# Kernel tuning notes

Measured on AMD Instinct MI355X. Metric: run time of the kernel, lower is better.

## Reference

```python
import jax, jax.numpy as jnp
import numpy as np

NUM_HEADS = 8
SIZES = [(80, 80), (40, 40), (20, 20), (10, 10), (5, 5)]


def _ln(x, g, b):
    m = x.mean(-1, keepdims=True)
    var = ((x - m) ** 2).mean(-1, keepdims=True)
    return (x - m) / jnp.sqrt(var + 1e-5) * g + b


def setup_inputs() -> dict:
    key = jax.random.key(0)
    ks = jax.random.split(key, 24)
    bs, c, S = 2, 256, 1024  # v_dim = embed_dim = c
    d = {}
    for i, (h, w) in enumerate(SIZES):
        d[f"q{i}"] = jax.random.normal(ks[i], (bs, c, h, w), jnp.float32)
    d["cache"] = jax.random.normal(ks[5], (bs, S, c), jnp.float32)
    d["mask"] = jax.random.randint(ks[6], (bs, S), 0, 2).astype(jnp.int32)
    d["ln_v_g"] = jnp.ones((c,), jnp.float32)
    d["ln_v_b"] = jnp.zeros((c,), jnp.float32)
    d["ln_c_g"] = jnp.ones((c,), jnp.float32)
    d["ln_c_b"] = jnp.zeros((c,), jnp.float32)
    sd = c ** -0.5
    d["Wv"] = jax.random.normal(ks[7], (c, c), jnp.float32) * sd
    d["bv"] = jnp.zeros((c,), jnp.float32)
    d["Wc"] = jax.random.normal(ks[8], (c, c), jnp.float32) * sd
    d["bc"] = jnp.zeros((c,), jnp.float32)
    d["Wvc"] = jax.random.normal(ks[9], (c, c), jnp.float32) * sd
    d["bvc"] = jnp.zeros((c,), jnp.float32)
    d["Wo"] = jax.random.normal(ks[10], (c, c), jnp.float32) * sd
    d["bo"] = jnp.zeros((c,), jnp.float32)
    d["Wg1"] = jax.random.normal(ks[11], (c, c // 2), jnp.float32) * sd
    d["bg1"] = jnp.zeros((c // 2,), jnp.float32)
    d["Wg2"] = jax.random.normal(ks[12], (c // 2, c), jnp.float32) * 0.01
    d["bg2"] = jnp.zeros((c,), jnp.float32)
    return d


def _forward(q0, q1, q2, q3, q4, cache, mask, ln_v_g, ln_v_b, ln_c_g, ln_c_b,
             Wv, bv, Wc, bc, Wvc, bvc, Wo, bo, Wg1, bg1, Wg2, bg2):
    feats = [q0, q1, q2, q3, q4]
    bs = q0.shape[0]
    sizes = [(f.shape[2], f.shape[3]) for f in feats]
    # permute_and_flatten: (bs, c, h, w) -> (bs, h*w, c), concat over levels
    v = jnp.concatenate(
        [f.reshape(bs, f.shape[1], -1).transpose(0, 2, 1) for f in feats], axis=1)
    T = v.shape[1]
    E = Wv.shape[1]
    hd = E // NUM_HEADS
    scale = hd ** -0.5

    vn = _ln(v, ln_v_g, ln_v_b)
    cn = _ln(cache, ln_c_g, ln_c_b)

    q = ((vn @ Wv + bv) * scale).reshape(bs, T, NUM_HEADS, hd).transpose(0, 2, 1, 3)
    k = (cn @ Wc + bc).reshape(bs, -1, NUM_HEADS, hd).transpose(0, 2, 1, 3)
    val = (cn @ Wvc + bvc).reshape(bs, -1, NUM_HEADS, hd).transpose(0, 2, 1, 3)

    attn = jnp.einsum('bhtd,bhsd->bhts', q, k)
    attn = jnp.clip(attn, -50000.0, 50000.0)
    mf = mask.astype(attn.dtype)  # (bs, S); zeros -> -9e15, ones kept as +1.0 (faithful)
    attn = attn + jnp.where(mf == 0, jnp.asarray(-9e15, attn.dtype), mf)[:, None, None, :]
    p = jax.nn.softmax(attn, axis=-1)  # dropout inactive in eval mode

    o = jnp.einsum('bhts,bhsd->bhtd', p, val).transpose(0, 2, 1, 3).reshape(bs, T, E)
    delta = o @ Wo + bo

    gate = jnp.tanh(jax.nn.relu(v @ Wg1 + bg1) @ Wg2 + bg2)
    new_v = (v + gate * delta).transpose(0, 2, 1)  # (bs, c, T)

    outs = []
    start = 0
    for h, w in sizes:
        outs.append(new_v[:, :, start:start + h * w].reshape(bs, -1, h, w))
        start += h * w
    return tuple(outs)


def reference(q0, q1, q2, q3, q4, cache, mask, ln_v_g, ln_v_b, ln_c_g, ln_c_b,
              Wv, bv, Wc, bc, Wvc, bvc, Wo, bo, Wg1, bg1, Wg2, bg2):
    return _forward(q0, q1, q2, q3, q4, cache, mask, ln_v_g, ln_v_b, ln_c_g, ln_c_b,
                    Wv, bv, Wc, bc, Wvc, bvc, Wo, bo, Wg1, bg1, Wg2, bg2)
```

## Files before the change

kernel.cpp:

```cpp
#include <hip/hip_runtime.h>
#include <hip/hip_bf16.h>
#include <math.h>


typedef __attribute__((ext_vector_type(8))) short short8;
typedef __attribute__((ext_vector_type(4))) float f32x4;
typedef __hip_bfloat16 bf16;

#define T_TOK 8525
#define S_TOK 1024
#define CDIM  256
#define NHEAD 8
#define BSZ   2

static __device__ __forceinline__ f32x4 mfma16(short8 a, short8 b, f32x4 c) {
  return __builtin_amdgcn_mfma_f32_16x16x32_bf16(a, b, c, 0, 0, 0);
}

__global__ __launch_bounds__(256) void prep_weights(
    const float* __restrict__ Wv, const float* __restrict__ Wc,
    const float* __restrict__ Wvc, const float* __restrict__ Wo,
    const float* __restrict__ Wg1, const float* __restrict__ Wg2,
    const float* __restrict__ bc, const float* __restrict__ bvc,
    bf16* __restrict__ WvT, bf16* __restrict__ WcvcT, bf16* __restrict__ WoT,
    bf16* __restrict__ Wg1T, bf16* __restrict__ Wg2T, float* __restrict__ biasCV) {
  const int bid = blockIdx.x, tid = threadIdx.x;
  if (bid >= 80) {
    biasCV[tid] = bc[tid];
    biasCV[tid + 256] = bvc[tid];
    return;
  }
  const float* W; bf16* WT; int K, N, local;
  if (bid < 16)      { W = Wv;  WT = WvT;           K = 256; N = 256; local = bid; }
  else if (bid < 32) { W = Wc;  WT = WcvcT;         K = 256; N = 256; local = bid - 16; }
  else if (bid < 48) { W = Wvc; WT = WcvcT + 65536; K = 256; N = 256; local = bid - 32; }
  else if (bid < 64) { W = Wo;  WT = WoT;           K = 256; N = 256; local = bid - 48; }
  else if (bid < 72) { W = Wg1; WT = Wg1T;          K = 256; N = 128; local = bid - 64; }
  else               { W = Wg2; WT = Wg2T;          K = 128; N = 256; local = bid - 72; }
  const int ktiles = K >> 6;
  const int K0 = (local % ktiles) * 64, N0 = (local / ktiles) * 64;
  __shared__ float tl[64][65];
  const int kk = tid >> 4, n4 = (tid & 15) * 4;
#pragma unroll
  for (int i = 0; i < 4; ++i) {
    int k = kk + 16 * i;
    float4 w4 = *(const float4*)&W[(size_t)(K0 + k) * N + N0 + n4];
    tl[n4 + 0][k] = w4.x; tl[n4 + 1][k] = w4.y;
    tl[n4 + 2][k] = w4.z; tl[n4 + 3][k] = w4.w;
  }
  __syncthreads();
  const int nn = tid >> 4, k4 = (tid & 15) * 4;
#pragma unroll
  for (int i = 0; i < 4; ++i) {
    int n = nn + 16 * i;
    bf16 o[4] __attribute__((aligned(8)));
#pragma unroll
    for (int j = 0; j < 4; ++j) o[j] = __float2bfloat16(tl[n][k4 + j]);
    *(uint2*)&WT[(size_t)(N0 + n) * K + K0 + k4] = *(uint2*)o;
  }
}

__global__ __launch_bounds__(256) void build_v_ln(
    const float* __restrict__ q0, const float* __restrict__ q1,
    const float* __restrict__ q2, const float* __restrict__ q3,
    const float* __restrict__ q4, const float* __restrict__ g,
    const float* __restrict__ beta, float* __restrict__ v,
    bf16* __restrict__ vb, bf16* __restrict__ vnb) {
  constexpr int HW[5] = {6400, 1600, 400, 100, 25};
  constexpr int TST[5] = {0, 6400, 8000, 8400, 8500};
  constexpr int T16[5] = {0, 400, 500, 525, 532};
  __shared__ float tile[16][260];
  const int tid = threadIdx.x;
  const int tileid = blockIdx.x, b = blockIdx.y;
  int lvl = 0;
#pragma unroll
  for (int i = 1; i < 5; ++i) if (tileid >= T16[i]) lvl = i;
  const int p0 = (tileid - T16[lvl]) * 16;
  const int hw = HW[lvl];
  const float* src = ((lvl == 0) ? q0 : (lvl == 1) ? q1 : (lvl == 2) ? q2
                      : (lvl == 3) ? q3 : q4) + (size_t)b * CDIM * hw;
  const int pl = tid & 15, cb = tid >> 4;
  const int pg = p0 + pl;
#pragma unroll
  for (int i = 0; i < 16; ++i) {
    int c = cb + 16 * i;
    tile[pl][c] = (pg < hw) ? src[(size_t)c * hw + pg] : 0.f;
  }
  __syncthreads();
  const int lane = tid & 63, w = tid >> 6;
#pragma unroll
  for (int rr = 0; rr < 4; ++rr) {
    int row = w * 4 + rr;
    int p = p0 + row;
    if (p >= hw) continue;
    float x0 = tile[row][lane], x1 = tile[row][lane + 64],
          x2 = tile[row][lane + 128], x3 = tile[row][lane + 192];
    float s = x0 + x1 + x2 + x3;
    float s2 = x0 * x0 + x1 * x1 + x2 * x2 + x3 * x3;
#pragma unroll
    for (int off = 1; off < 64; off <<= 1) {
      s += __shfl_xor(s, off);
      s2 += __shfl_xor(s2, off);
    }
    float mean = s * (1.f / 256.f);
    float var = s2 * (1.f / 256.f) - mean * mean;
    float rstd = rsqrtf(var + 1e-5f);
    size_t base = ((size_t)b * T_TOK + TST[lvl] + p) * CDIM;
    float xs[4] = {x0, x1, x2, x3};
#pragma unroll
    for (int j = 0; j < 4; ++j) {
      int c = lane + 64 * j;
      float x = xs[j];
      v[base + c] = x;
      vb[base + c] = __float2bfloat16(x);
      vnb[base + c] = __float2bfloat16((x - mean) * rstd * g[c] + beta[c]);
    }
  }
}

__global__ __launch_bounds__(256) void ln_rows(
    const float* __restrict__ X, const float* __restrict__ g,
    const float* __restrict__ bta, bf16* __restrict__ Y, int nrows) {
  int lane = threadIdx.x & 63;
  int row = blockIdx.x * 4 + (threadIdx.x >> 6);
  if (row >= nrows) return;
  const float* x = X + (size_t)row * CDIM;
  float v0 = x[lane], v1 = x[lane + 64], v2 = x[lane + 128], v3 = x[lane + 192];
  float s = v0 + v1 + v2 + v3;
  float s2 = v0 * v0 + v1 * v1 + v2 * v2 + v3 * v3;
#pragma unroll
  for (int off = 1; off < 64; off <<= 1) {
    s += __shfl_xor(s, off);
    s2 += __shfl_xor(s2, off);
  }
  float mean = s * (1.f / 256.f);
  float var = s2 * (1.f / 256.f) - mean * mean;
  float rstd = rsqrtf(var + 1e-5f);
  bf16* y = Y + (size_t)row * CDIM;
  y[lane] = __float2bfloat16((v0 - mean) * rstd * g[lane] + bta[lane]);
  y[lane + 64] = __float2bfloat16((v1 - mean) * rstd * g[lane + 64] + bta[lane + 64]);
  y[lane + 128] = __float2bfloat16((v2 - mean) * rstd * g[lane + 128] + bta[lane + 128]);
  y[lane + 192] = __float2bfloat16((v3 - mean) * rstd * g[lane + 192] + bta[lane + 192]);
}

template <int K, int EPI>
__global__ __launch_bounds__(256) void gemm_nt(
    const bf16* __restrict__ A, const bf16* __restrict__ WT,
    const float* __restrict__ bias, void* __restrict__ out,
    float* __restrict__ auxD, int M) {
  __shared__ __align__(16) bf16 Asl[128][136];
  __shared__ __align__(16) bf16 Bsl[64][136];
  const int tid = threadIdx.x;
  const int wave = tid >> 6, lane = tid & 63, quad = lane >> 4, l15 = lane & 15;
  const int m0 = blockIdx.y * 128;
  const int n0 = blockIdx.x * 64;
  f32x4 acc[2][4];
#pragma unroll
  for (int i = 0; i < 2; ++i)
#pragma unroll
    for (int j = 0; j < 4; ++j) acc[i][j] = (f32x4){0.f, 0.f, 0.f, 0.f};

  for (int k0 = 0; k0 < K; k0 += 128) {
    __syncthreads();
#pragma unroll
    for (int c = 0; c < 8; ++c) {
      int chunk = c * 256 + tid;
      int row = chunk >> 4, col = (chunk & 15) * 8;
      int gr = m0 + row;
      if (gr >= M) gr = M - 1;
      *(uint4*)&Asl[row][col] = *(const uint4*)&A[(size_t)gr * K + k0 + col];
    }
#pragma unroll
    for (int c = 0; c < 4; ++c) {
      int chunk = c * 256 + tid;
      int row = chunk >> 4, col = (chunk & 15) * 8;
      *(uint4*)&Bsl[row][col] = *(const uint4*)&WT[(size_t)(n0 + row) * K + k0 + col];
    }
    __syncthreads();
#pragma unroll
    for (int kk = 0; kk < 128; kk += 32) {
      short8 af0 = *(const short8*)&Asl[wave * 32 + l15][kk + quad * 8];
      short8 af1 = *(const short8*)&Asl[wave * 32 + 16 + l15][kk + quad * 8];
      short8 bf0 = *(const short8*)&Bsl[l15][kk + quad * 8];
      short8 bf1 = *(const short8*)&Bsl[16 + l15][kk + quad * 8];
      short8 bf2 = *(const short8*)&Bsl[32 + l15][kk + quad * 8];
      short8 bf3 = *(const short8*)&Bsl[48 + l15][kk + quad * 8];
      acc[0][0] = mfma16(af0, bf0, acc[0][0]);
      acc[0][1] = mfma16(af0, bf1, acc[0][1]);
      acc[0][2] = mfma16(af0, bf2, acc[0][2]);
      acc[0][3] = mfma16(af0, bf3, acc[0][3]);
      acc[1][0] = mfma16(af1, bf0, acc[1][0]);
      acc[1][1] = mfma16(af1, bf1, acc[1][1]);
      acc[1][2] = mfma16(af1, bf2, acc[1][2]);
      acc[1][3] = mfma16(af1, bf3, acc[1][3]);
    }
  }
  const int ldN = gridDim.x * 64;
#pragma unroll
  for (int ms = 0; ms < 2; ++ms)
#pragma unroll
    for (int nt = 0; nt < 4; ++nt)
#pragma unroll
      for (int r = 0; r < 4; ++r) {
        int m = m0 + wave * 32 + ms * 16 + quad * 4 + r;
        if (m >= M) continue;
        int n = n0 + nt * 16 + l15;
        float x = acc[ms][nt][r] + bias[n];
        if (EPI == 0) {
          ((bf16*)out)[(size_t)m * ldN + n] =
              __float2bfloat16(x * 0.17677669529663687f);
        } else if (EPI == 4) {
          ((bf16*)out)[(size_t)m * ldN + n] = __float2bfloat16(fmaxf(x, 0.f));
        } else {
          if (n < 256) {
            ((bf16*)out)[(size_t)m * 256 + n] = __float2bfloat16(x);
          } else {
            int n2 = n - 256;
            int bb = m >> 10, s = m & 1023;
            int hh = n2 >> 5, d = n2 & 31;
            ((bf16*)auxD)[(((size_t)(bb * NHEAD + hh) * 32 + d) << 10) + s] =
                __float2bfloat16(x);
          }
        }
      }
}

__global__ __launch_bounds__(512) void attn_kernel(
    const bf16* __restrict__ qb, const bf16* __restrict__ kb,
    const bf16* __restrict__ valTb, const int* __restrict__ mask,
    bf16* __restrict__ ob) {
  __shared__ __align__(16) bf16 Ksl[2][128][40];
  __shared__ __align__(16) bf16 Vsl[2][4096];
  __shared__ __align__(16) float biasl[2][128];
  const int tid = threadIdx.x;
  const int wv = tid >> 6, lane = tid & 63, quad = lane >> 4, l15 = lane & 15;
  const int b = blockIdx.y >> 3, h = blockIdx.y & 7;
  const int t0w = blockIdx.x * 128 + wv * 16;
  int t_load = t0w + l15;
  if (t_load >= T_TOK) t_load = T_TOK - 1;
  short8 qf = *(const short8*)&qb[((size_t)b * T_TOK + t_load) * CDIM + h * 32 + quad * 8];
  f32x4 o0 = (f32x4){0.f, 0.f, 0.f, 0.f};
  f32x4 o1 = (f32x4){0.f, 0.f, 0.f, 0.f};
  float lsum = 0.f;
  const f32x4 zero4 = (f32x4){0.f, 0.f, 0.f, 0.f};
  const size_t kbase = ((size_t)b * S_TOK) * CDIM + h * 32;
  const size_t vbase = (size_t)(b * NHEAD + h) << 15;
  const int ks = tid >> 2, kd = (tid & 3) * 8;
  const int vd = tid >> 4, vs8 = (tid & 15) * 8;
  const int P0tab[4] = {0, 16, 4, 20};
  const int p1 = (vs8 >> 5) * 32 + P0tab[(vs8 >> 3) & 3];
  const int p2 = p1 + 8;
  const int vx = vd & 7;
  const int vo1 = vd * 128 + (((p1 >> 3) ^ vx) << 3) + (p1 & 7);
  const int vo2 = vd * 128 + (((p2 >> 3) ^ vx) << 3) + (p2 & 7);
  const int rx = l15 & 7;

  uint4 kreg = *(const uint4*)&kb[kbase + (size_t)ks * CDIM + kd];
  uint4 vreg = *(const uint4*)&valTb[vbase + ((size_t)vd << 10) + vs8];
  float breg = 0.f;
  if (tid < 128) breg = mask[b * S_TOK + tid] ? -9.0f : -9e15f;
  *(uint4*)&Ksl[0][ks][kd] = kreg;
  {
    uint2 lo = {kreg.x, kreg.x};
    lo.x = vreg.x; lo.y = vreg.y;
    uint2 hi; hi.x = vreg.z; hi.y = vreg.w;
    *(uint2*)&Vsl[0][vo1] = lo;
    *(uint2*)&Vsl[0][vo2] = hi;
  }
  if (tid < 128) biasl[0][tid] = breg;
  __syncthreads();

  for (int sbi = 0; sbi < 8; ++sbi) {
    const int cur = sbi & 1;
    if (sbi < 7) {
      int sb = (sbi + 1) * 128;
      kreg = *(const uint4*)&kb[kbase + (size_t)(sb + ks) * CDIM + kd];
      vreg = *(const uint4*)&valTb[vbase + ((size_t)vd << 10) + sb + vs8];
      if (tid < 128) breg = mask[b * S_TOK + sb + tid] ? -9.0f : -9e15f;
    }
#pragma unroll
    for (int ss = 0; ss < 128; ss += 32) {
      short8 kf0 = *(const short8*)&Ksl[cur][ss + l15][quad * 8];
      short8 kf1 = *(const short8*)&Ksl[cur][ss + 16 + l15][quad * 8];
      f32x4 s0 = mfma16(kf0, qf, zero4);
      f32x4 s1 = mfma16(kf1, qf, zero4);
      float4 bb0 = *(const float4*)&biasl[cur][ss + quad * 4];
      float4 bb1 = *(const float4*)&biasl[cur][ss + 16 + quad * 4];
      float pa = __expf(s0[0] + bb0.x), pb = __expf(s0[1] + bb0.y);
      float pc = __expf(s0[2] + bb0.z), pd = __expf(s0[3] + bb0.w);
      float pe = __expf(s1[0] + bb1.x), pf_ = __expf(s1[1] + bb1.y);
      float pg = __expf(s1[2] + bb1.z), ph = __expf(s1[3] + bb1.w);
      lsum += ((pa + pb) + (pc + pd)) + ((pe + pf_) + (pg + ph));
      unsigned int u0 = (__float_as_uint(pa) >> 16) | (__float_as_uint(pb) & 0xFFFF0000u);
      unsigned int u1 = (__float_as_uint(pc) >> 16) | (__float_as_uint(pd) & 0xFFFF0000u);
      unsigned int u2 = (__float_as_uint(pe) >> 16) | (__float_as_uint(pf_) & 0xFFFF0000u);
      unsigned int u3 = (__float_as_uint(pg) >> 16) | (__float_as_uint(ph) & 0xFFFF0000u);
      uint4 pu; pu.x = u0; pu.y = u1; pu.z = u2; pu.w = u3;
      short8 pfr = *(short8*)&pu;
      int vc = (ss >> 3) + quad;
      short8 vf0 = *(const short8*)&Vsl[cur][l15 * 128 + ((vc ^ rx) << 3)];
      short8 vf1 = *(const short8*)&Vsl[cur][(16 + l15) * 128 + ((vc ^ rx) << 3)];
      o0 = mfma16(pfr, vf0, o0);
      o1 = mfma16(pfr, vf1, o1);
    }
    if (sbi < 7) {
      const int nxt = cur ^ 1;
      *(uint4*)&Ksl[nxt][ks][kd] = kreg;
      uint2 lo; lo.x = vreg.x; lo.y = vreg.y;
      uint2 hi; hi.x = vreg.z; hi.y = vreg.w;
      *(uint2*)&Vsl[nxt][vo1] = lo;
      *(uint2*)&Vsl[nxt][vo2] = hi;
      if (tid < 128) biasl[nxt][tid] = breg;
    }
    __syncthreads();
  }
  lsum += __shfl_xor(lsum, 16);
  lsum += __shfl_xor(lsum, 32);
#pragma unroll
  for (int r = 0; r < 4; ++r) {
    int tl = quad * 4 + r;
    float rli = 1.0f / __shfl(lsum, tl);
    int t = t0w + tl;
    if (t < T_TOK) {
      size_t basep = ((size_t)b * T_TOK + t) * CDIM + h * 32;
      ob[basep + l15] = __float2bfloat16(o0[r] * rli);
      ob[basep + 16 + l15] = __float2bfloat16(o1[r] * rli);
    }
  }
}

__global__ __launch_bounds__(256) void gemm_out(
    const bf16* __restrict__ obuf, const bf16* __restrict__ WoT,
    const float* __restrict__ bo, const bf16* __restrict__ ghb,
    const bf16* __restrict__ Wg2T, const float* __restrict__ bg2,
    const float* __restrict__ v, float* __restrict__ out, int M) {
  constexpr int HW[5] = {6400, 1600, 400, 100, 25};
  constexpr int TST[5] = {0, 6400, 8000, 8400, 8500};
  constexpr size_t OUTOFF[5] = {0, 3276800, 4096000, 4300800, 4352000};
  __shared__ __align__(16) bf16 Asl[128][136];
  __shared__ __align__(16) bf16 Bsl[64][136];
  const int tid = threadIdx.x;
  const int wave = tid >> 6, lane = tid & 63, quad = lane >> 4, l15 = lane & 15;
  const int m0 = blockIdx.y * 128, n0 = blockIdx.x * 64;
  f32x4 aD[4][2], aG[4][2];
#pragma unroll
  for (int j = 0; j < 4; ++j)
#pragma unroll
    for (int i = 0; i < 2; ++i) {
      aD[j][i] = (f32x4){0.f, 0.f, 0.f, 0.f};
      aG[j][i] = (f32x4){0.f, 0.f, 0.f, 0.f};
    }
  for (int k0 = 0; k0 < 256; k0 += 128) {
    __syncthreads();
#pragma unroll
    for (int c = 0; c < 8; ++c) {
      int chunk = c * 256 + tid;
      int row = chunk >> 4, col = (chunk & 15) * 8;
      int gr = m0 + row;
      if (gr >= M) gr = M - 1;
      *(uint4*)&Asl[row][col] = *(const uint4*)&obuf[(size_t)gr * 256 + k0 + col];
    }
#pragma unroll
    for (int c = 0; c < 4; ++c) {
      int chunk = c * 256 + tid;
      int row = chunk >> 4, col = (chunk & 15) * 8;
      *(uint4*)&Bsl[row][col] = *(const uint4*)&WoT[(size_t)(n0 + row) * 256 + k0 + col];
    }
    __syncthreads();
#pragma unroll
    for (int kk = 0; kk < 128; kk += 32) {
      short8 af0 = *(const short8*)&Asl[wave * 32 + l15][kk + quad * 8];
      short8 af1 = *(const short8*)&Asl[wave * 32 + 16 + l15][kk + quad * 8];
#pragma unroll
      for (int j = 0; j < 4; ++j) {
        short8 bfj = *(const short8*)&Bsl[j * 16 + l15][kk + quad * 8];
        aD[j][0] = mfma16(bfj, af0, aD[j][0]);
        aD[j][1] = mfma16(bfj, af1, aD[j][1]);
      }
    }
  }
  __syncthreads();
#pragma unroll
  for (int c = 0; c < 8; ++c) {
    int chunk = c * 256 + tid;
    int row = chunk >> 4, col = (chunk & 15) * 8;
    int gr = m0 + row;
    if (gr >= M) gr = M - 1;
    *(uint4*)&Asl[row][col] = *(const uint4*)&ghb[(size_t)gr * 128 + col];
  }
#pragma unroll
  for (int c = 0; c < 4; ++c) {
    int chunk = c * 256 + tid;
    int row = chunk >> 4, col = (chunk & 15) * 8;
    *(uint4*)&Bsl[row][col] = *(const uint4*)&Wg2T[(size_t)(n0 + row) * 128 + col];
  }
  __syncthreads();
#pragma unroll
  for (int kk = 0; kk < 128; kk += 32) {
    short8 af0 = *(const short8*)&Asl[wave * 32 + l15][kk + quad * 8];
    short8 af1 = *(const short8*)&Asl[wave * 32 + 16 + l15][kk + quad * 8];
#pragma unroll
    for (int j = 0; j < 4; ++j) {
      short8 bfj = *(const short8*)&Bsl[j * 16 + l15][kk + quad * 8];
      aG[j][0] = mfma16(bfj, af0, aG[j][0]);
      aG[j][1] = mfma16(bfj, af1, aG[j][1]);
    }
  }
#pragma unroll
  for (int ms = 0; ms < 2; ++ms) {
    int t = m0 + wave * 32 + ms * 16 + l15;
    if (t >= M) continue;
    int bb = (t >= T_TOK) ? 1 : 0;
    int tt = t - bb * T_TOK;
    int lvl = 0;
#pragma unroll
    for (int i = 1; i < 5; ++i) if (tt >= TST[i]) lvl = i;
    int p = tt - TST[lvl], hw = HW[lvl];
    float* dst = out + OUTOFF[lvl] + (size_t)bb * CDIM * hw + p;
    const float* vrow = v + (size_t)t * CDIM;
#pragma unroll
    for (int nt = 0; nt < 4; ++nt) {
      float4 bo4 = *(const float4*)&bo[n0 + nt * 16 + quad * 4];
      float4 bg4 = *(const float4*)&bg2[n0 + nt * 16 + quad * 4];
      float bod[4] = {bo4.x, bo4.y, bo4.z, bo4.w};
      float bgd[4] = {bg4.x, bg4.y, bg4.z, bg4.w};
#pragma unroll
      for (int r = 0; r < 4; ++r) {
        int c = n0 + nt * 16 + quad * 4 + r;
        float xd = aD[nt][ms][r] + bod[r];
        float xg = aG[nt][ms][r] + bgd[r];
        float xc = fminf(fmaxf(xg, -15.f), 15.f);
        float e = __expf(2.f * xc);
        float gt = (e - 1.f) / (e + 1.f);
        dst[(size_t)c * hw] = vrow[c] + gt * xd;
      }
    }
  }
}

extern "C" void kernel_launch(void* const* d_in, const int* in_sizes, int n_in,
                              void* d_out, int out_size, void* d_ws, size_t ws_size,
                              hipStream_t stream) {
  const float* q0 = (const float*)d_in[0];
  const float* q1 = (const float*)d_in[1];
  const float* q2 = (const float*)d_in[2];
  const float* q3 = (const float*)d_in[3];
  const float* q4 = (const float*)d_in[4];
  const float* cache = (const float*)d_in[5];
  const int* mask = (const int*)d_in[6];
  const float* ln_v_g = (const float*)d_in[7];
  const float* ln_v_b = (const float*)d_in[8];
  const float* ln_c_g = (const float*)d_in[9];
  const float* ln_c_b = (const float*)d_in[10];
  const float* Wv = (const float*)d_in[11];
  const float* bv = (const float*)d_in[12];
  const float* Wc = (const float*)d_in[13];
  const float* bc = (const float*)d_in[14];
  const float* Wvc = (const float*)d_in[15];
  const float* bvc = (const float*)d_in[16];
  const float* Wo = (const float*)d_in[17];
  const float* bo = (const float*)d_in[18];
  const float* Wg1 = (const float*)d_in[19];
  const float* bg1 = (const float*)d_in[20];
  const float* Wg2 = (const float*)d_in[21];
  const float* bg2 = (const float*)d_in[22];
  float* out = (float*)d_out;

  const int R = BSZ * T_TOK;
  const size_t RC = (size_t)R * CDIM;
  const size_t SC = (size_t)BSZ * S_TOK * CDIM;

  char* p = (char*)d_ws;
  float* v_f32 = (float*)p;        p += RC * 4;
  bf16* vb = (bf16*)p;             p += RC * 2;
  bf16* vnb = (bf16*)p;            p += RC * 2;
  bf16* qb = (bf16*)p;             p += RC * 2;
  bf16* ob = (bf16*)p;             p += RC * 2;
  bf16* ghb = (bf16*)p;            p += (size_t)R * 128 * 2;
  bf16* cnb = (bf16*)p;            p += SC * 2;
  bf16* kb = (bf16*)p;             p += SC * 2;
  bf16* valTb = (bf16*)p;          p += SC * 2;
  bf16* WvT = (bf16*)p;            p += 65536 * 2;
  bf16* WcvcT = (bf16*)p;          p += 131072 * 2;
  bf16* WoT = (bf16*)p;            p += 65536 * 2;
  bf16* Wg1T = (bf16*)p;           p += 32768 * 2;
  bf16* Wg2T = (bf16*)p;           p += 32768 * 2;
  float* biasCV = (float*)p;       p += 512 * 4;

  prep_weights<<<dim3(81), dim3(256), 0, stream>>>(
      Wv, Wc, Wvc, Wo, Wg1, Wg2, bc, bvc, WvT, WcvcT, WoT, Wg1T, Wg2T, biasCV);
  build_v_ln<<<dim3(534, BSZ), dim3(256), 0, stream>>>(
      q0, q1, q2, q3, q4, ln_v_g, ln_v_b, v_f32, vb, vnb);
  ln_rows<<<dim3(512), dim3(256), 0, stream>>>(cache, ln_c_g, ln_c_b, cnb, BSZ * S_TOK);
  gemm_nt<256, 0><<<dim3(4, 134), dim3(256), 0, stream>>>(
      vnb, WvT, bv, qb, nullptr, R);
  gemm_nt<256, 6><<<dim3(8, 16), dim3(256), 0, stream>>>(
      cnb, WcvcT, biasCV, kb, (float*)valTb, BSZ * S_TOK);
  gemm_nt<256, 4><<<dim3(2, 134), dim3(256), 0, stream>>>(
      vb, Wg1T, bg1, ghb, nullptr, R);
  attn_kernel<<<dim3(67, BSZ * NHEAD), dim3(512), 0, stream>>>(
      qb, kb, valTb, mask, ob);
  gemm_out<<<dim3(4, 134), dim3(256), 0, stream>>>(
      ob, WoT, bo, ghb, Wg2T, bg2, v_f32, out, R);
}
```

Baseline: 239.4 us.

## Fuse cache LN into prep, use exp2 softmax with MFMA row-sum, coalesce output stores

The cache layernorm moves into the weight-prep kernel, which removes one launch. Attention now folds log2(e) into the q scale and the mask bias, and feeds the bias into the MFMA accumulator so it can use raw exp2. The row sum comes from an extra MFMA against a ones vector instead of shuffles. The K tile gets a new LDS layout. The output GEMM stages its result through LDS and reads v from a channel-major copy so the NCHW stores are coalesced, at the cost of an extra transposed write in build_v_ln.

```diff
diff --git a/kernel.cpp b/kernel.cpp
--- a/kernel.cpp
+++ b/kernel.cpp
@@ -17,17 +17,58 @@
   return __builtin_amdgcn_mfma_f32_16x16x32_bf16(a, b, c, 0, 0, 0);
 }
 
-__global__ __launch_bounds__(256) void prep_weights(
+static __device__ __forceinline__ float fexp2(float x) {
+#if __has_builtin(__builtin_amdgcn_exp2f)
+  return __builtin_amdgcn_exp2f(x);
+#else
+  return exp2f(x);
+#endif
+}
+
+static __device__ __forceinline__ unsigned int pack_bf16(float a, float b) {
+#if __has_builtin(__builtin_amdgcn_perm)
+  return __builtin_amdgcn_perm(__float_as_uint(b), __float_as_uint(a), 0x07060302u);
+#else
+  return (__float_as_uint(a) >> 16) | (__float_as_uint(b) & 0xFFFF0000u);
+#endif
+}
+
+__global__ __launch_bounds__(256) void prep_misc(
     const float* __restrict__ Wv, const float* __restrict__ Wc,
     const float* __restrict__ Wvc, const float* __restrict__ Wo,
     const float* __restrict__ Wg1, const float* __restrict__ Wg2,
     const float* __restrict__ bc, const float* __restrict__ bvc,
+    const float* __restrict__ cache, const float* __restrict__ ln_c_g,
+    const float* __restrict__ ln_c_b,
     bf16* __restrict__ WvT, bf16* __restrict__ WcvcT, bf16* __restrict__ WoT,
-    bf16* __restrict__ Wg1T, bf16* __restrict__ Wg2T, float* __restrict__ biasCV) {
+    bf16* __restrict__ Wg1T, bf16* __restrict__ Wg2T, float* __restrict__ biasCV,
+    bf16* __restrict__ cnb) {
   const int bid = blockIdx.x, tid = threadIdx.x;
-  if (bid >= 80) {
+  if (bid == 80) {
     biasCV[tid] = bc[tid];
     biasCV[tid + 256] = bvc[tid];
+    return;
+  }
+  if (bid > 80) {
+    int lane = tid & 63;
+    int row = (bid - 81) * 4 + (tid >> 6);
+    const float* x = cache + (size_t)row * CDIM;
+    float v0 = x[lane], v1 = x[lane + 64], v2 = x[lane + 128], v3 = x[lane + 192];
+    float s = v0 + v1 + v2 + v3;
+    float s2 = v0 * v0 + v1 * v1 + v2 * v2 + v3 * v3;
+#pragma unroll
+    for (int off = 1; off < 64; off <<= 1) {
+      s += __shfl_xor(s, off);
+      s2 += __shfl_xor(s2, off);
+    }
+    float mean = s * (1.f / 256.f);
+    float var = s2 * (1.f / 256.f) - mean * mean;
+    float rstd = rsqrtf(var + 1e-5f);
+    bf16* y = cnb + (size_t)row * CDIM;
+    y[lane] = __float2bfloat16((v0 - mean) * rstd * ln_c_g[lane] + ln_c_b[lane]);
+    y[lane + 64] = __float2bfloat16((v1 - mean) * rstd * ln_c_g[lane + 64] + ln_c_b[lane + 64]);
+    y[lane + 128] = __float2bfloat16((v2 - mean) * rstd * ln_c_g[lane + 128] + ln_c_b[lane + 128]);
+    y[lane + 192] = __float2bfloat16((v3 - mean) * rstd * ln_c_g[lane + 192] + ln_c_b[lane + 192]);
     return;
   }
   const float* W; bf16* WT; int K, N, local;
@@ -64,7 +105,7 @@
     const float* __restrict__ q0, const float* __restrict__ q1,
     const float* __restrict__ q2, const float* __restrict__ q3,
     const float* __restrict__ q4, const float* __restrict__ g,
-    const float* __restrict__ beta, float* __restrict__ v,
+    const float* __restrict__ beta, float* __restrict__ vT,
     bf16* __restrict__ vb, bf16* __restrict__ vnb) {
   constexpr int HW[5] = {6400, 1600, 400, 100, 25};
   constexpr int TST[5] = {0, 6400, 8000, 8400, 8500};
@@ -87,6 +128,14 @@
     tile[pl][c] = (pg < hw) ? src[(size_t)c * hw + pg] : 0.f;
   }
   __syncthreads();
+  if (pg < hw) {
+    int tglob = TST[lvl] + pg;
+#pragma unroll
+    for (int i = 0; i < 16; ++i) {
+      int c = cb + 16 * i;
+      vT[((size_t)b * CDIM + c) * T_TOK + tglob] = tile[pl][c];
+    }
+  }
   const int lane = tid & 63, w = tid >> 6;
 #pragma unroll
   for (int rr = 0; rr < 4; ++rr) {
@@ -111,36 +160,10 @@
     for (int j = 0; j < 4; ++j) {
       int c = lane + 64 * j;
       float x = xs[j];
-      v[base + c] = x;
       vb[base + c] = __float2bfloat16(x);
       vnb[base + c] = __float2bfloat16((x - mean) * rstd * g[c] + beta[c]);
     }
   }
-}
-
-__global__ __launch_bounds__(256) void ln_rows(
-    const float* __restrict__ X, const float* __restrict__ g,
-    const float* __restrict__ bta, bf16* __restrict__ Y, int nrows) {
-  int lane = threadIdx.x & 63;
-  int row = blockIdx.x * 4 + (threadIdx.x >> 6);
-  if (row >= nrows) return;
-  const float* x = X + (size_t)row * CDIM;
-  float v0 = x[lane], v1 = x[lane + 64], v2 = x[lane + 128], v3 = x[lane + 192];
-  float s = v0 + v1 + v2 + v3;
-  float s2 = v0 * v0 + v1 * v1 + v2 * v2 + v3 * v3;
-#pragma unroll
-  for (int off = 1; off < 64; off <<= 1) {
-    s += __shfl_xor(s, off);
-    s2 += __shfl_xor(s2, off);
-  }
-  float mean = s * (1.f / 256.f);
-  float var = s2 * (1.f / 256.f) - mean * mean;
-  float rstd = rsqrtf(var + 1e-5f);
-  bf16* y = Y + (size_t)row * CDIM;
-  y[lane] = __float2bfloat16((v0 - mean) * rstd * g[lane] + bta[lane]);
-  y[lane + 64] = __float2bfloat16((v1 - mean) * rstd * g[lane + 64] + bta[lane + 64]);
-  y[lane + 128] = __float2bfloat16((v2 - mean) * rstd * g[lane + 128] + bta[lane + 128]);
-  y[lane + 192] = __float2bfloat16((v3 - mean) * rstd * g[lane + 192] + bta[lane + 192]);
 }
 
 template <int K, int EPI>
@@ -207,8 +230,7 @@
         int n = n0 + nt * 16 + l15;
         float x = acc[ms][nt][r] + bias[n];
         if (EPI == 0) {
-          ((bf16*)out)[(size_t)m * ldN + n] =
-              __float2bfloat16(x * 0.17677669529663687f);
+          ((bf16*)out)[(size_t)m * ldN + n] = __float2bfloat16(x * 0.25504765517f);
         } else if (EPI == 4) {
           ((bf16*)out)[(size_t)m * ldN + n] = __float2bfloat16(fmaxf(x, 0.f));
         } else {
@@ -229,7 +251,7 @@
     const bf16* __restrict__ qb, const bf16* __restrict__ kb,
     const bf16* __restrict__ valTb, const int* __restrict__ mask,
     bf16* __restrict__ ob) {
-  __shared__ __align__(16) bf16 Ksl[2][128][40];
+  __shared__ __align__(16) bf16 Ksl[2][4096];
   __shared__ __align__(16) bf16 Vsl[2][4096];
   __shared__ __align__(16) float biasl[2][128];
   const int tid = threadIdx.x;
@@ -241,11 +263,13 @@
   short8 qf = *(const short8*)&qb[((size_t)b * T_TOK + t_load) * CDIM + h * 32 + quad * 8];
   f32x4 o0 = (f32x4){0.f, 0.f, 0.f, 0.f};
   f32x4 o1 = (f32x4){0.f, 0.f, 0.f, 0.f};
-  float lsum = 0.f;
-  const f32x4 zero4 = (f32x4){0.f, 0.f, 0.f, 0.f};
+  f32x4 o2 = (f32x4){0.f, 0.f, 0.f, 0.f};
+  const short8 ones = (short8){0x3F80, 0x3F80, 0x3F80, 0x3F80,
+                               0x3F80, 0x3F80, 0x3F80, 0x3F80};
   const size_t kbase = ((size_t)b * S_TOK) * CDIM + h * 32;
   const size_t vbase = (size_t)(b * NHEAD + h) << 15;
-  const int ks = tid >> 2, kd = (tid & 3) * 8;
+  const int ks = tid >> 2, kd16 = tid & 3;
+  const int kdst = (ks >> 4) * 512 + (ks & 15) * 32 + kd16 * 8;
   const int vd = tid >> 4, vs8 = (tid & 15) * 8;
   const int P0tab[4] = {0, 16, 4, 20};
   const int p1 = (vs8 >> 5) * 32 + P0tab[(vs8 >> 3) & 3];
@@ -255,14 +279,13 @@
   const int vo2 = vd * 128 + (((p2 >> 3) ^ vx) << 3) + (p2 & 7);
   const int rx = l15 & 7;
 
-  uint4 kreg = *(const uint4*)&kb[kbase + (size_t)ks * CDIM + kd];
+  uint4 kreg = *(const uint4*)&kb[kbase + (size_t)ks * CDIM + kd16 * 8];
   uint4 vreg = *(const uint4*)&valTb[vbase + ((size_t)vd << 10) + vs8];
   float breg = 0.f;
-  if (tid < 128) breg = mask[b * S_TOK + tid] ? -9.0f : -9e15f;
-  *(uint4*)&Ksl[0][ks][kd] = kreg;
+  if (tid < 128) breg = mask[b * S_TOK + tid] ? -12.984255368f : -1e18f;
+  *(uint4*)&Ksl[0][kdst] = kreg;
   {
-    uint2 lo = {kreg.x, kreg.x};
-    lo.x = vreg.x; lo.y = vreg.y;
+    uint2 lo; lo.x = vreg.x; lo.y = vreg.y;
     uint2 hi; hi.x = vreg.z; hi.y = vreg.w;
     *(uint2*)&Vsl[0][vo1] = lo;
     *(uint2*)&Vsl[0][vo2] = hi;
@@ -274,38 +297,38 @@
     const int cur = sbi & 1;
     if (sbi < 7) {
       int sb = (sbi + 1) * 128;
-      kreg = *(const uint4*)&kb[kbase + (size_t)(sb + ks) * CDIM + kd];
+      kreg = *(const uint4*)&kb[kbase + (size_t)(sb + ks) * CDIM + kd16 * 8];
       vreg = *(const uint4*)&valTb[vbase + ((size_t)vd << 10) + sb + vs8];
-      if (tid < 128) breg = mask[b * S_TOK + sb + tid] ? -9.0f : -9e15f;
+      if (tid < 128) breg = mask[b * S_TOK + sb + tid] ? -12.984255368f : -1e18f;
     }
 #pragma unroll
     for (int ss = 0; ss < 128; ss += 32) {
-      short8 kf0 = *(const short8*)&Ksl[cur][ss + l15][quad * 8];
-      short8 kf1 = *(const short8*)&Ksl[cur][ss + 16 + l15][quad * 8];
-      f32x4 s0 = mfma16(kf0, qf, zero4);
-      f32x4 s1 = mfma16(kf1, qf, zero4);
-      float4 bb0 = *(const float4*)&biasl[cur][ss + quad * 4];
-      float4 bb1 = *(const float4*)&biasl[cur][ss + 16 + quad * 4];
-      float pa = __expf(s0[0] + bb0.x), pb = __expf(s0[1] + bb0.y);
-      float pc = __expf(s0[2] + bb0.z), pd = __expf(s0[3] + bb0.w);
-      float pe = __expf(s1[0] + bb1.x), pf_ = __expf(s1[1] + bb1.y);
-      float pg = __expf(s1[2] + bb1.z), ph = __expf(s1[3] + bb1.w);
-      lsum += ((pa + pb) + (pc + pd)) + ((pe + pf_) + (pg + ph));
-      unsigned int u0 = (__float_as_uint(pa) >> 16) | (__float_as_uint(pb) & 0xFFFF0000u);
-      unsigned int u1 = (__float_as_uint(pc) >> 16) | (__float_as_uint(pd) & 0xFFFF0000u);
-      unsigned int u2 = (__float_as_uint(pe) >> 16) | (__float_as_uint(pf_) & 0xFFFF0000u);
-      unsigned int u3 = (__float_as_uint(pg) >> 16) | (__float_as_uint(ph) & 0xFFFF0000u);
-      uint4 pu; pu.x = u0; pu.y = u1; pu.z = u2; pu.w = u3;
+      short8 kf0 = *(const short8*)&Ksl[cur][(ss >> 4) * 512 + l15 * 32 + quad * 8];
+      short8 kf1 = *(const short8*)&Ksl[cur][(ss >> 4) * 512 + 512 + l15 * 32 + quad * 8];
+      f32x4 bias0 = *(const f32x4*)&biasl[cur][ss + quad * 4];
+      f32x4 bias1 = *(const f32x4*)&biasl[cur][ss + 16 + quad * 4];
+      f32x4 s0 = mfma16(kf0, qf, bias0);
+      f32x4 s1 = mfma16(kf1, qf, bias1);
+      float pa = fexp2(s0[0]), pb = fexp2(s0[1]);
+      float pc = fexp2(s0[2]), pd = fexp2(s0[3]);
+      float pe = fexp2(s1[0]), pf_ = fexp2(s1[1]);
+      float pg = fexp2(s1[2]), ph = fexp2(s1[3]);
+      uint4 pu;
+      pu.x = pack_bf16(pa, pb);
+      pu.y = pack_bf16(pc, pd);
+      pu.z = pack_bf16(pe, pf_);
+      pu.w = pack_bf16(pg, ph);
       short8 pfr = *(short8*)&pu;
       int vc = (ss >> 3) + quad;
       short8 vf0 = *(const short8*)&Vsl[cur][l15 * 128 + ((vc ^ rx) << 3)];
       short8 vf1 = *(const short8*)&Vsl[cur][(16 + l15) * 128 + ((vc ^ rx) << 3)];
+      o2 = mfma16(pfr, ones, o2);
       o0 = mfma16(pfr, vf0, o0);
       o1 = mfma16(pfr, vf1, o1);
     }
     if (sbi < 7) {
       const int nxt = cur ^ 1;
-      *(uint4*)&Ksl[nxt][ks][kd] = kreg;
+      *(uint4*)&Ksl[nxt][kdst] = kreg;
       uint2 lo; lo.x = vreg.x; lo.y = vreg.y;
       uint2 hi; hi.x = vreg.z; hi.y = vreg.w;
       *(uint2*)&Vsl[nxt][vo1] = lo;
@@ -314,14 +337,11 @@
     }
     __syncthreads();
   }
-  lsum += __shfl_xor(lsum, 16);
-  lsum += __shfl_xor(lsum, 32);
 #pragma unroll
   for (int r = 0; r < 4; ++r) {
-    int tl = quad * 4 + r;
-    float rli = 1.0f / __shfl(lsum, tl);
-    int t = t0w + tl;
+    int t = t0w + quad * 4 + r;
     if (t < T_TOK) {
+      float rli = 1.0f / o2[r];
       size_t basep = ((size_t)b * T_TOK + t) * CDIM + h * 32;
       ob[basep + l15] = __float2bfloat16(o0[r] * rli);
       ob[basep + 16 + l15] = __float2bfloat16(o1[r] * rli);
@@ -333,22 +353,24 @@
     const bf16* __restrict__ obuf, const bf16* __restrict__ WoT,
     const float* __restrict__ bo, const bf16* __restrict__ ghb,
     const bf16* __restrict__ Wg2T, const float* __restrict__ bg2,
-    const float* __restrict__ v, float* __restrict__ out, int M) {
+    const float* __restrict__ vT, float* __restrict__ out, int M) {
   constexpr int HW[5] = {6400, 1600, 400, 100, 25};
   constexpr int TST[5] = {0, 6400, 8000, 8400, 8500};
   constexpr size_t OUTOFF[5] = {0, 3276800, 4096000, 4300800, 4352000};
-  __shared__ __align__(16) bf16 Asl[128][136];
-  __shared__ __align__(16) bf16 Bsl[64][136];
+  __shared__ __align__(16) char smem[52224];
+  bf16 (*Asl)[136] = (bf16(*)[136])smem;
+  bf16 (*Bsl)[136] = (bf16(*)[136])(smem + 34816);
+  float (*tile)[132] = (float(*)[132])smem;
   const int tid = threadIdx.x;
   const int wave = tid >> 6, lane = tid & 63, quad = lane >> 4, l15 = lane & 15;
   const int m0 = blockIdx.y * 128, n0 = blockIdx.x * 64;
-  f32x4 aD[4][2], aG[4][2];
-#pragma unroll
-  for (int j = 0; j < 4; ++j)
-#pragma unroll
-    for (int i = 0; i < 2; ++i) {
-      aD[j][i] = (f32x4){0.f, 0.f, 0.f, 0.f};
-      aG[j][i] = (f32x4){0.f, 0.f, 0.f, 0.f};
+  f32x4 aD[2][4], aG[2][4];
+#pragma unroll
+  for (int i = 0; i < 2; ++i)
+#pragma unroll
+    for (int j = 0; j < 4; ++j) {
+      aD[i][j] = (f32x4){0.f, 0.f, 0.f, 0.f};
+      aG[i][j] = (f32x4){0.f, 0.f, 0.f, 0.f};
     }
   for (int k0 = 0; k0 < 256; k0 += 128) {
     __syncthreads();
@@ -374,8 +396,8 @@
 #pragma unroll
       for (int j = 0; j < 4; ++j) {
         short8 bfj = *(const short8*)&Bsl[j * 16 + l15][kk + quad * 8];
-        aD[j][0] = mfma16(bfj, af0, aD[j][0]);
-        aD[j][1] = mfma16(bfj, af1, aD[j][1]);
+        aD[0][j] = mfma16(af0, bfj, aD[0][j]);
+        aD[1][j] = mfma16(af1, bfj, aD[1][j]);
       }
     }
   }
@@ -402,39 +424,48 @@
 #pragma unroll
     for (int j = 0; j < 4; ++j) {
       short8 bfj = *(const short8*)&Bsl[j * 16 + l15][kk + quad * 8];
-      aG[j][0] = mfma16(bfj, af0, aG[j][0]);
-      aG[j][1] = mfma16(bfj, af1, aG[j][1]);
-    }
-  }
-#pragma unroll
-  for (int ms = 0; ms < 2; ++ms) {
-    int t = m0 + wave * 32 + ms * 16 + l15;
-    if (t >= M) continue;
-    int bb = (t >= T_TOK) ? 1 : 0;
-    int tt = t - bb * T_TOK;
-    int lvl = 0;
-#pragma unroll
-    for (int i = 1; i < 5; ++i) if (tt >= TST[i]) lvl = i;
-    int p = tt - TST[lvl], hw = HW[lvl];
-    float* dst = out + OUTOFF[lvl] + (size_t)bb * CDIM * hw + p;
-    const float* vrow = v + (size_t)t * CDIM;
+      aG[0][j] = mfma16(af0, bfj, aG[0][j]);
+      aG[1][j] = mfma16(af1, bfj, aG[1][j]);
+    }
+  }
+  __syncthreads();
+#pragma unroll
+  for (int ms = 0; ms < 2; ++ms)
 #pragma unroll
     for (int nt = 0; nt < 4; ++nt) {
-      float4 bo4 = *(const float4*)&bo[n0 + nt * 16 + quad * 4];
-      float4 bg4 = *(const float4*)&bg2[n0 + nt * 16 + quad * 4];
-      float bod[4] = {bo4.x, bo4.y, bo4.z, bo4.w};
-      float bgd[4] = {bg4.x, bg4.y, bg4.z, bg4.w};
+      int n = n0 + nt * 16 + l15;
+      float bod = bo[n], bgd = bg2[n];
+      float4 res;
+      float tmp[4];
 #pragma unroll
       for (int r = 0; r < 4; ++r) {
-        int c = n0 + nt * 16 + quad * 4 + r;
-        float xd = aD[nt][ms][r] + bod[r];
-        float xg = aG[nt][ms][r] + bgd[r];
+        float xd = aD[ms][nt][r] + bod;
+        float xg = aG[ms][nt][r] + bgd;
         float xc = fminf(fmaxf(xg, -15.f), 15.f);
         float e = __expf(2.f * xc);
         float gt = (e - 1.f) / (e + 1.f);
-        dst[(size_t)c * hw] = vrow[c] + gt * xd;
+        tmp[r] = gt * xd;
       }
-    }
+      res.x = tmp[0]; res.y = tmp[1]; res.z = tmp[2]; res.w = tmp[3];
+      *(float4*)&tile[nt * 16 + l15][wave * 32 + ms * 16 + quad * 4] = res;
+    }
+  __syncthreads();
+  const int tl = tid & 127, c2 = tid >> 7;
+  const int t = m0 + tl;
+  const bool valid = t < M;
+  int bb = (t >= T_TOK) ? 1 : 0;
+  int tt = t - bb * T_TOK;
+  if (tt >= T_TOK) tt = T_TOK - 1;
+  int lvl = 0;
+#pragma unroll
+  for (int i = 1; i < 5; ++i) if (tt >= TST[i]) lvl = i;
+  const int p = tt - TST[lvl], hw = HW[lvl];
+  float* dst = out + OUTOFF[lvl] + ((size_t)bb * CDIM + n0) * hw + p;
+  const float* vsrc = vT + ((size_t)bb * CDIM + n0) * T_TOK + tt;
+#pragma unroll
+  for (int c0 = 0; c0 < 32; ++c0) {
+    int c = c0 * 2 + c2;
+    if (valid) dst[(size_t)c * hw] = vsrc[(size_t)c * T_TOK] + tile[c][tl];
   }
 }
 
@@ -471,7 +502,7 @@
   const size_t SC = (size_t)BSZ * S_TOK * CDIM;
 
   char* p = (char*)d_ws;
-  float* v_f32 = (float*)p;        p += RC * 4;
+  float* vT = (float*)p;           p += RC * 4;
   bf16* vb = (bf16*)p;             p += RC * 2;
   bf16* vnb = (bf16*)p;            p += RC * 2;
   bf16* qb = (bf16*)p;             p += RC * 2;
@@ -487,11 +518,11 @@
   bf16* Wg2T = (bf16*)p;           p += 32768 * 2;
   float* biasCV = (float*)p;       p += 512 * 4;
 
-  prep_weights<<<dim3(81), dim3(256), 0, stream>>>(
-      Wv, Wc, Wvc, Wo, Wg1, Wg2, bc, bvc, WvT, WcvcT, WoT, Wg1T, Wg2T, biasCV);
+  prep_misc<<<dim3(593), dim3(256), 0, stream>>>(
+      Wv, Wc, Wvc, Wo, Wg1, Wg2, bc, bvc, cache, ln_c_g, ln_c_b,
+      WvT, WcvcT, WoT, Wg1T, Wg2T, biasCV, cnb);
   build_v_ln<<<dim3(534, BSZ), dim3(256), 0, stream>>>(
-      q0, q1, q2, q3, q4, ln_v_g, ln_v_b, v_f32, vb, vnb);
-  ln_rows<<<dim3(512), dim3(256), 0, stream>>>(cache, ln_c_g, ln_c_b, cnb, BSZ * S_TOK);
+      q0, q1, q2, q3, q4, ln_v_g, ln_v_b, vT, vb, vnb);
   gemm_nt<256, 0><<<dim3(4, 134), dim3(256), 0, stream>>>(
       vnb, WvT, bv, qb, nullptr, R);
   gemm_nt<256, 6><<<dim3(8, 16), dim3(256), 0, stream>>>(
@@ -501,5 +532,5 @@
   attn_kernel<<<dim3(67, BSZ * NHEAD), dim3(512), 0, stream>>>(
       qb, kb, valTb, mask, ob);
   gemm_out<<<dim3(4, 134), dim3(256), 0, stream>>>(
-      ob, WoT, bo, ghb, Wg2T, bg2, v_f32, out, R);
-}
+      ob, WoT, bo, ghb, Wg2T, bg2, vT, out, R);
+}
```

Result: faster. 216.7 us (-9.5%).
